# Kernel optimization log

Measured on AMD Instinct MI355X. Metric: run time of the kernel, lower is better.

## Reference

```python
import jax, jax.numpy as jnp
import numpy as np

N = 16384
E = 65536

def _nnconv(x, src, dst, edge_attr, A, b, root, bias, c_in, c_out):
    # edge MLP: [E,2] -> [E, c_in*c_out], ReLU
    W = jax.nn.relu(edge_attr @ A + b).reshape(E, c_in, c_out)
    # gather source features, per-edge matmul: [E,c_in] x [E,c_in,c_out] -> [E,c_out]
    msg = jnp.einsum('ei,eio->eo', x[src], W)
    # scatter-add to target nodes
    agg = jax.ops.segment_sum(msg, dst, num_segments=N)
    return agg + x @ root + bias

def setup_inputs() -> dict:
    key = jax.random.key(0)
    ks = jax.random.split(key, 12)
    inp = {
        'x': jax.random.normal(ks[0], (N, 8), dtype=jnp.float32),
        'edge_index': jax.random.randint(ks[1], (2, E), 0, N, dtype=jnp.int64),
        'edge_attr': jax.random.normal(ks[2], (E, 2), dtype=jnp.float32),
        # edge-MLP 1: Linear(2, 512)
        'A1': jax.random.normal(ks[3], (2, 512), dtype=jnp.float32) * (1.0 / np.sqrt(2.0)),
        'b1': jnp.zeros((512,), dtype=jnp.float32),
        # edge-MLP 2: Linear(2, 4096)
        'A2': jax.random.normal(ks[4], (2, 4096), dtype=jnp.float32) * (1.0 / np.sqrt(2.0)),
        'b2': jnp.zeros((4096,), dtype=jnp.float32),
        # NNConv root weights + biases
        'root1': jax.random.normal(ks[5], (8, 64), dtype=jnp.float32) * (1.0 / np.sqrt(8.0)),
        'bias1': jnp.zeros((64,), dtype=jnp.float32),
        'root2': jax.random.normal(ks[6], (64, 64), dtype=jnp.float32) * (1.0 / np.sqrt(64.0)),
        'bias2': jnp.zeros((64,), dtype=jnp.float32),
    }
    return inp

def reference(x, edge_index, edge_attr, A1, b1, A2, b2, root1, bias1, root2, bias2):
    src = edge_index[0]  # x_j (message source)
    dst = edge_index[1]  # aggregation target
    h = _nnconv(x, src, dst, edge_attr, A1, b1, root1, bias1, 8, 64)
    h = _nnconv(h, src, dst, edge_attr, A2, b2, root2, bias2, 64, 64)
    return h
```

## Files before the change

### kernel.cpp

```cpp
#include <hip/hip_runtime.h>

#define N_NODES 16384
#define N_EDGES 65536

typedef float f32x16 __attribute__((ext_vector_type(16)));
typedef float f32x8  __attribute__((ext_vector_type(8)));
typedef float f32x4  __attribute__((ext_vector_type(4)));
typedef float f32x2  __attribute__((ext_vector_type(2)));

__device__ __forceinline__ float rfl_f(float v) {
    int i = __builtin_amdgcn_readfirstlane(__builtin_bit_cast(int, v));
    return __builtin_bit_cast(float, i);
}

__global__ void k_node1(const float* __restrict__ x, const float* __restrict__ root1,
                        const float* __restrict__ bias1, float* __restrict__ h1) {
    int t = blockIdx.x * blockDim.x + threadIdx.x;
    int n = t >> 6, o = t & 63;
    float acc = bias1[o];
#pragma unroll
    for (int i = 0; i < 8; ++i)
        acc = fmaf(x[n * 8 + i], root1[i * 64 + o], acc);
    h1[t] = acc;
}

__global__ __launch_bounds__(256)
void k_edge1(const float* __restrict__ x, const int* __restrict__ ei,
             const float* __restrict__ ea, const float* __restrict__ A1,
             const float* __restrict__ b1, float* __restrict__ h1) {
    int lane = threadIdx.x & 63;
    f32x8 W0, W1, BB;
#pragma unroll
    for (int i = 0; i < 8; ++i) {
        W0[i] = A1[i * 64 + lane];
        W1[i] = A1[512 + i * 64 + lane];
        BB[i] = b1[i * 64 + lane];
    }
    asm volatile("" : "+v"(W0), "+v"(W1), "+v"(BB));

    int wid = blockIdx.x * (blockDim.x >> 6) + (threadIdx.x >> 6);
    int nw = gridDim.x * (blockDim.x >> 6);
#pragma clang loop unroll(disable)
    for (int p = wid; p < N_EDGES / 2; p += nw) {
        int2 srcp = ((const int2*)ei)[p];
        int2 dstp = ((const int2*)(ei + N_EDGES))[p];
        float4 eap = ((const float4*)ea)[p];
        int s0 = __builtin_amdgcn_readfirstlane(srcp.x);
        int s1 = __builtin_amdgcn_readfirstlane(srcp.y);
        int d0 = __builtin_amdgcn_readfirstlane(dstp.x);
        int d1 = __builtin_amdgcn_readfirstlane(dstp.y);
        f32x2 e00 = {rfl_f(eap.x), rfl_f(eap.x)};
        f32x2 e01 = {rfl_f(eap.y), rfl_f(eap.y)};
        f32x2 e10 = {rfl_f(eap.z), rfl_f(eap.z)};
        f32x2 e11 = {rfl_f(eap.w), rfl_f(eap.w)};
        const float* xp0 = x + (size_t)s0 * 8;
        const float* xp1 = x + (size_t)s1 * 8;
        f32x8 ha, hb;
        asm volatile("s_load_dwordx8 %0, %2, 0x0\n\t"
                     "s_load_dwordx8 %1, %3, 0x0\n\t"
                     "s_waitcnt lgkmcnt(0)"
                     : "=&s"(ha), "=&s"(hb) : "s"(xp0), "s"(xp1));
        f32x2 acc0 = {0.f, 0.f}, acc1 = {0.f, 0.f};
        const f32x2 z2 = {0.f, 0.f};
#pragma unroll
        for (int k = 0; k < 4; ++k) {
            f32x2 w0p = {W0[2 * k], W0[2 * k + 1]};
            f32x2 w1p = {W1[2 * k], W1[2 * k + 1]};
            f32x2 bp  = {BB[2 * k], BB[2 * k + 1]};
            f32x2 wv0 = __builtin_elementwise_max(
                __builtin_elementwise_fma(e01, w1p,
                    __builtin_elementwise_fma(e00, w0p, bp)), z2);
            f32x2 h0p = {ha[2 * k], ha[2 * k + 1]};
            acc0 = __builtin_elementwise_fma(h0p, wv0, acc0);
            f32x2 wv1 = __builtin_elementwise_max(
                __builtin_elementwise_fma(e11, w1p,
                    __builtin_elementwise_fma(e10, w0p, bp)), z2);
            f32x2 h1p = {hb[2 * k], hb[2 * k + 1]};
            acc1 = __builtin_elementwise_fma(h1p, wv1, acc1);
        }
        atomicAdd(&h1[(size_t)d0 * 64 + lane], acc0[0] + acc0[1]);
        atomicAdd(&h1[(size_t)d1 * 64 + lane], acc1[0] + acc1[1]);
    }
}

__global__ __launch_bounds__(256)
void k_node2(const float* __restrict__ h1, const float* __restrict__ root2,
             const float* __restrict__ bias2, float* __restrict__ out) {
    int lane = threadIdx.x & 63;
    f32x16 R0, R1, R2, R3;
#pragma unroll
    for (int i = 0; i < 16; ++i) {
        R0[i] = root2[(i)      * 64 + lane];
        R1[i] = root2[(16 + i) * 64 + lane];
        R2[i] = root2[(32 + i) * 64 + lane];
        R3[i] = root2[(48 + i) * 64 + lane];
    }
    asm volatile("" : "+v"(R0), "+v"(R1), "+v"(R2), "+v"(R3));
    float bias = bias2[lane];

    int wid = blockIdx.x * (blockDim.x >> 6) + (threadIdx.x >> 6);
    int nw = gridDim.x * (blockDim.x >> 6);
#pragma clang loop unroll(disable)
    for (int n = wid; n < N_NODES; n += nw) {
        int nu = __builtin_amdgcn_readfirstlane(n);
        const float* hp = h1 + (size_t)nu * 64;
        f32x16 h0, h1v, h2, h3;
        asm volatile("s_load_dwordx16 %0, %4, 0x0\n\t"
                     "s_load_dwordx16 %1, %4, 0x40\n\t"
                     "s_load_dwordx16 %2, %4, 0x80\n\t"
                     "s_load_dwordx16 %3, %4, 0xc0\n\t"
                     "s_waitcnt lgkmcnt(0)"
                     : "=&s"(h0), "=&s"(h1v), "=&s"(h2), "=&s"(h3) : "s"(hp));
        f32x2 accp = {bias, 0.f};
#pragma unroll
        for (int k = 0; k < 8; ++k) {
            f32x2 hp0 = {h0[2 * k], h0[2 * k + 1]};
            f32x2 rp0 = {R0[2 * k], R0[2 * k + 1]};
            accp = __builtin_elementwise_fma(hp0, rp0, accp);
            f32x2 hp1 = {h1v[2 * k], h1v[2 * k + 1]};
            f32x2 rp1 = {R1[2 * k], R1[2 * k + 1]};
            accp = __builtin_elementwise_fma(hp1, rp1, accp);
            f32x2 hp2 = {h2[2 * k], h2[2 * k + 1]};
            f32x2 rp2 = {R2[2 * k], R2[2 * k + 1]};
            accp = __builtin_elementwise_fma(hp2, rp2, accp);
            f32x2 hp3 = {h3[2 * k], h3[2 * k + 1]};
            f32x2 rp3 = {R3[2 * k], R3[2 * k + 1]};
            accp = __builtin_elementwise_fma(hp3, rp3, accp);
        }
        out[(size_t)nu * 64 + lane] = accp[0] + accp[1];
    }
}

__global__ __launch_bounds__(256, 3)
void k_edge2(const float* __restrict__ h1, const int* __restrict__ ei,
             const float* __restrict__ ea, const float* __restrict__ A2,
             const float* __restrict__ b2, float* __restrict__ out) {
    __shared__ __align__(16) float WT[3 * 64 * 36];
    int half = blockIdx.x & 1;
    for (int j = threadIdx.x; j < 2048; j += 256) {
        int i = j >> 6, o = j & 63;
        WT[o * 36 + i]               = A2[half * 2048 + j];
        WT[64 * 36 + o * 36 + i]     = A2[4096 + half * 2048 + j];
        WT[2 * 64 * 36 + o * 36 + i] = b2[half * 2048 + j];
    }
    __syncthreads();

    int lane = threadIdx.x & 63;
    int base = __builtin_amdgcn_readfirstlane(half * 32);
    unsigned laddr = (unsigned)(uintptr_t)WT + lane * 144;

    f32x4 wa[8], wb[8], wc[8];
    asm volatile(
        "ds_read_b128 %0, %12 offset:0\n\t"
        "ds_read_b128 %1, %12 offset:16\n\t"
        "ds_read_b128 %2, %12 offset:32\n\t"
        "ds_read_b128 %3, %12 offset:48\n\t"
        "ds_read_b128 %4, %12 offset:9216\n\t"
        "ds_read_b128 %5, %12 offset:9232\n\t"
        "ds_read_b128 %6, %12 offset:9248\n\t"
        "ds_read_b128 %7, %12 offset:9264\n\t"
        "ds_read_b128 %8, %12 offset:18432\n\t"
        "ds_read_b128 %9, %12 offset:18448\n\t"
        "ds_read_b128 %10, %12 offset:18464\n\t"
        "ds_read_b128 %11, %12 offset:18480"
        : "=&v"(wa[0]), "=&v"(wa[1]), "=&v"(wa[2]), "=&v"(wa[3]),
          "=&v"(wb[0]), "=&v"(wb[1]), "=&v"(wb[2]), "=&v"(wb[3]),
          "=&v"(wc[0]), "=&v"(wc[1]), "=&v"(wc[2]), "=&v"(wc[3])
        : "v"(laddr));
    asm volatile(
        "ds_read_b128 %0, %12 offset:64\n\t"
        "ds_read_b128 %1, %12 offset:80\n\t"
        "ds_read_b128 %2, %12 offset:96\n\t"
        "ds_read_b128 %3, %12 offset:112\n\t"
        "ds_read_b128 %4, %12 offset:9280\n\t"
        "ds_read_b128 %5, %12 offset:9296\n\t"
        "ds_read_b128 %6, %12 offset:9312\n\t"
        "ds_read_b128 %7, %12 offset:9328\n\t"
        "ds_read_b128 %8, %12 offset:18496\n\t"
        "ds_read_b128 %9, %12 offset:18512\n\t"
        "ds_read_b128 %10, %12 offset:18528\n\t"
        "ds_read_b128 %11, %12 offset:18544"
        : "=&v"(wa[4]), "=&v"(wa[5]), "=&v"(wa[6]), "=&v"(wa[7]),
          "=&v"(wb[4]), "=&v"(wb[5]), "=&v"(wb[6]), "=&v"(wb[7]),
          "=&v"(wc[4]), "=&v"(wc[5]), "=&v"(wc[6]), "=&v"(wc[7])
        : "v"(laddr));
    asm volatile("s_waitcnt lgkmcnt(0)"
        : "+v"(wa[0]), "+v"(wa[1]), "+v"(wa[2]), "+v"(wa[3]),
          "+v"(wa[4]), "+v"(wa[5]), "+v"(wa[6]), "+v"(wa[7]),
          "+v"(wb[0]), "+v"(wb[1]), "+v"(wb[2]), "+v"(wb[3]),
          "+v"(wb[4]), "+v"(wb[5]), "+v"(wb[6]), "+v"(wb[7]),
          "+v"(wc[0]), "+v"(wc[1]), "+v"(wc[2]), "+v"(wc[3]),
          "+v"(wc[4]), "+v"(wc[5]), "+v"(wc[6]), "+v"(wc[7]));

    int g = blockIdx.x >> 1;
    int wslot = g * 4 + (threadIdx.x >> 6);
    const int STRIDE = 1536;

    f32x16 ha, hb, hc, hd;

    int p0 = wslot;
    int2   dst_c = ((const int2*)(ei + N_EDGES))[p0];
    float4 ea_c  = ((const float4*)ea)[p0];
    {
        int2 src0 = ((const int2*)ei)[p0];
        int s0 = __builtin_amdgcn_readfirstlane(src0.x);
        int s1 = __builtin_amdgcn_readfirstlane(src0.y);
        const float* hp0 = h1 + (size_t)s0 * 64 + base;
        const float* hp1 = h1 + (size_t)s1 * 64 + base;
        asm volatile("s_load_dwordx16 %0, %4, 0x0\n\t"
                     "s_load_dwordx16 %1, %4, 0x40\n\t"
                     "s_load_dwordx16 %2, %5, 0x0\n\t"
                     "s_load_dwordx16 %3, %5, 0x40"
                     : "=&s"(ha), "=&s"(hb), "=&s"(hc), "=&s"(hd)
                     : "s"(hp0), "s"(hp1));
    }
    int pn = p0 + STRIDE; if (pn > N_EDGES / 2 - 1) pn = N_EDGES / 2 - 1;
    int2   src_n = ((const int2*)ei)[pn];
    int2   dst_n = ((const int2*)(ei + N_EDGES))[pn];
    float4 ea_n  = ((const float4*)ea)[pn];

#pragma clang loop unroll(disable)
    for (int p = wslot; p < N_EDGES / 2; p += STRIDE) {
        int s0n = __builtin_amdgcn_readfirstlane(src_n.x);
        int s1n = __builtin_amdgcn_readfirstlane(src_n.y);
        const float* hpn0 = h1 + (size_t)s0n * 64 + base;
        const float* hpn1 = h1 + (size_t)s1n * 64 + base;

        asm volatile("s_waitcnt lgkmcnt(0)"
            : "+s"(ha), "+s"(hb), "+s"(hc), "+s"(hd));

        f32x2 e00 = {ea_c.x, ea_c.x}, e01 = {ea_c.y, ea_c.y};
        f32x2 e10 = {ea_c.z, ea_c.z}, e11 = {ea_c.w, ea_c.w};
        const f32x2 z2 = {0.f, 0.f};
        f32x2 acc0 = z2, acc1 = z2;
#pragma unroll
        for (int q = 0; q < 4; ++q) {
#pragma unroll
            for (int k = 0; k < 2; ++k) {
                f32x2 w0p = {wa[q][2 * k], wa[q][2 * k + 1]};
                f32x2 w1p = {wb[q][2 * k], wb[q][2 * k + 1]};
                f32x2 bp  = {wc[q][2 * k], wc[q][2 * k + 1]};
                f32x2 wv0 = __builtin_elementwise_max(
                    __builtin_elementwise_fma(e01, w1p,
                        __builtin_elementwise_fma(e00, w0p, bp)), z2);
                f32x2 h0p = {ha[q * 4 + 2 * k], ha[q * 4 + 2 * k + 1]};
                acc0 = __builtin_elementwise_fma(h0p, wv0, acc0);
                f32x2 wv1 = __builtin_elementwise_max(
                    __builtin_elementwise_fma(e11, w1p,
                        __builtin_elementwise_fma(e10, w0p, bp)), z2);
                f32x2 h1p = {hc[q * 4 + 2 * k], hc[q * 4 + 2 * k + 1]};
                acc1 = __builtin_elementwise_fma(h1p, wv1, acc1);
            }
        }
        asm volatile("s_load_dwordx16 %0, %2, 0x0\n\t"
                     "s_load_dwordx16 %1, %3, 0x0"
                     : "=&s"(ha), "=&s"(hc) : "s"(hpn0), "s"(hpn1));
#pragma unroll
        for (int q = 4; q < 8; ++q) {
#pragma unroll
            for (int k = 0; k < 2; ++k) {
                f32x2 w0p = {wa[q][2 * k], wa[q][2 * k + 1]};
                f32x2 w1p = {wb[q][2 * k], wb[q][2 * k + 1]};
                f32x2 bp  = {wc[q][2 * k], wc[q][2 * k + 1]};
                f32x2 wv0 = __builtin_elementwise_max(
                    __builtin_elementwise_fma(e01, w1p,
                        __builtin_elementwise_fma(e00, w0p, bp)), z2);
                f32x2 h0p = {hb[(q - 4) * 4 + 2 * k], hb[(q - 4) * 4 + 2 * k + 1]};
                acc0 = __builtin_elementwise_fma(h0p, wv0, acc0);
                f32x2 wv1 = __builtin_elementwise_max(
                    __builtin_elementwise_fma(e11, w1p,
                        __builtin_elementwise_fma(e10, w0p, bp)), z2);
                f32x2 h1p = {hd[(q - 4) * 4 + 2 * k], hd[(q - 4) * 4 + 2 * k + 1]};
                acc1 = __builtin_elementwise_fma(h1p, wv1, acc1);
            }
        }
        asm volatile("s_load_dwordx16 %0, %2, 0x40\n\t"
                     "s_load_dwordx16 %1, %3, 0x40"
                     : "=&s"(hb), "=&s"(hd) : "s"(hpn0), "s"(hpn1));

        atomicAdd(&out[(size_t)dst_c.x * 64 + lane], acc0[0] + acc0[1]);
        atomicAdd(&out[(size_t)dst_c.y * 64 + lane], acc1[0] + acc1[1]);

        dst_c = dst_n; ea_c = ea_n;
        int pn2 = p + 2 * STRIDE; if (pn2 > N_EDGES / 2 - 1) pn2 = N_EDGES / 2 - 1;
        src_n = ((const int2*)ei)[pn2];
        dst_n = ((const int2*)(ei + N_EDGES))[pn2];
        ea_n  = ((const float4*)ea)[pn2];
    }
}

extern "C" void kernel_launch(void* const* d_in, const int* in_sizes, int n_in,
                              void* d_out, int out_size, void* d_ws, size_t ws_size,
                              hipStream_t stream) {
    const float* x     = (const float*)d_in[0];
    const int*   ei    = (const int*)d_in[1];
    const float* ea    = (const float*)d_in[2];
    const float* A1    = (const float*)d_in[3];
    const float* b1    = (const float*)d_in[4];
    const float* A2    = (const float*)d_in[5];
    const float* b2    = (const float*)d_in[6];
    const float* root1 = (const float*)d_in[7];
    const float* bias1 = (const float*)d_in[8];
    const float* root2 = (const float*)d_in[9];
    const float* bias2 = (const float*)d_in[10];
    float* out = (float*)d_out;
    float* h1  = (float*)d_ws;

    k_node1<<<N_NODES * 64 / 256, 256, 0, stream>>>(x, root1, bias1, h1);
    k_edge1<<<2048, 256, 0, stream>>>(x, ei, ea, A1, b1, h1);
    k_node2<<<1024, 256, 0, stream>>>(h1, root2, bias2, out);
    k_edge2<<<768, 256, 0, stream>>>(h1, ei, ea, A2, b2, out);
}
```

Measured before the change: 137.8 us.

## Software-pipeline edge1/node2 loads and split edge2 input channels into quarters

k_edge1 and k_node2 now prefetch the next iteration's indices and gathered scalar features before the current compute, so the scalar-load wait overlaps with arithmetic and atomics. k_edge2 splits the 64 input channels into four 16-channel slices per block instead of two 32-channel halves. This halves the per-wave weight registers and LDS footprint, drops the occupancy hint, and raises the grid to 2048 blocks. The price is twice as many atomic adds into the output and more redundant index and edge-attribute loads per edge.

```diff
diff --git a/kernel.cpp b/kernel.cpp
--- a/kernel.cpp
+++ b/kernel.cpp
@@ -40,28 +40,39 @@
 
     int wid = blockIdx.x * (blockDim.x >> 6) + (threadIdx.x >> 6);
     int nw = gridDim.x * (blockDim.x >> 6);
+
+    f32x8 ha, hb;
+    int p0 = wid;
+    int2   dst_c = ((const int2*)(ei + N_EDGES))[p0];
+    float4 ea_c  = ((const float4*)ea)[p0];
+    {
+        int2 s = ((const int2*)ei)[p0];
+        int s0 = __builtin_amdgcn_readfirstlane(s.x);
+        int s1 = __builtin_amdgcn_readfirstlane(s.y);
+        const float* xp0 = x + (size_t)s0 * 8;
+        const float* xp1 = x + (size_t)s1 * 8;
+        asm volatile("s_load_dwordx8 %0, %2, 0x0\n\t"
+                     "s_load_dwordx8 %1, %3, 0x0"
+                     : "=&s"(ha), "=&s"(hb) : "s"(xp0), "s"(xp1));
+    }
+    int pn = p0 + nw; if (pn > N_EDGES / 2 - 1) pn = N_EDGES / 2 - 1;
+    int2   src_n = ((const int2*)ei)[pn];
+    int2   dst_n = ((const int2*)(ei + N_EDGES))[pn];
+    float4 ea_n  = ((const float4*)ea)[pn];
+
 #pragma clang loop unroll(disable)
     for (int p = wid; p < N_EDGES / 2; p += nw) {
-        int2 srcp = ((const int2*)ei)[p];
-        int2 dstp = ((const int2*)(ei + N_EDGES))[p];
-        float4 eap = ((const float4*)ea)[p];
-        int s0 = __builtin_amdgcn_readfirstlane(srcp.x);
-        int s1 = __builtin_amdgcn_readfirstlane(srcp.y);
-        int d0 = __builtin_amdgcn_readfirstlane(dstp.x);
-        int d1 = __builtin_amdgcn_readfirstlane(dstp.y);
-        f32x2 e00 = {rfl_f(eap.x), rfl_f(eap.x)};
-        f32x2 e01 = {rfl_f(eap.y), rfl_f(eap.y)};
-        f32x2 e10 = {rfl_f(eap.z), rfl_f(eap.z)};
-        f32x2 e11 = {rfl_f(eap.w), rfl_f(eap.w)};
-        const float* xp0 = x + (size_t)s0 * 8;
-        const float* xp1 = x + (size_t)s1 * 8;
-        f32x8 ha, hb;
-        asm volatile("s_load_dwordx8 %0, %2, 0x0\n\t"
-                     "s_load_dwordx8 %1, %3, 0x0\n\t"
-                     "s_waitcnt lgkmcnt(0)"
-                     : "=&s"(ha), "=&s"(hb) : "s"(xp0), "s"(xp1));
-        f32x2 acc0 = {0.f, 0.f}, acc1 = {0.f, 0.f};
+        int s0n = __builtin_amdgcn_readfirstlane(src_n.x);
+        int s1n = __builtin_amdgcn_readfirstlane(src_n.y);
+        const float* xpn0 = x + (size_t)s0n * 8;
+        const float* xpn1 = x + (size_t)s1n * 8;
+
+        asm volatile("s_waitcnt lgkmcnt(0)" : "+s"(ha), "+s"(hb));
+
+        f32x2 e00 = {ea_c.x, ea_c.x}, e01 = {ea_c.y, ea_c.y};
+        f32x2 e10 = {ea_c.z, ea_c.z}, e11 = {ea_c.w, ea_c.w};
         const f32x2 z2 = {0.f, 0.f};
+        f32x2 acc0 = z2, acc1 = z2;
 #pragma unroll
         for (int k = 0; k < 4; ++k) {
             f32x2 w0p = {W0[2 * k], W0[2 * k + 1]};
@@ -78,8 +89,18 @@
             f32x2 h1p = {hb[2 * k], hb[2 * k + 1]};
             acc1 = __builtin_elementwise_fma(h1p, wv1, acc1);
         }
-        atomicAdd(&h1[(size_t)d0 * 64 + lane], acc0[0] + acc0[1]);
-        atomicAdd(&h1[(size_t)d1 * 64 + lane], acc1[0] + acc1[1]);
+        asm volatile("s_load_dwordx8 %0, %2, 0x0\n\t"
+                     "s_load_dwordx8 %1, %3, 0x0"
+                     : "=&s"(ha), "=&s"(hb) : "s"(xpn0), "s"(xpn1));
+
+        atomicAdd(&h1[(size_t)dst_c.x * 64 + lane], acc0[0] + acc0[1]);
+        atomicAdd(&h1[(size_t)dst_c.y * 64 + lane], acc1[0] + acc1[1]);
+
+        dst_c = dst_n; ea_c = ea_n;
+        int pn2 = p + 2 * nw; if (pn2 > N_EDGES / 2 - 1) pn2 = N_EDGES / 2 - 1;
+        src_n = ((const int2*)ei)[pn2];
+        dst_n = ((const int2*)(ei + N_EDGES))[pn2];
+        ea_n  = ((const float4*)ea)[pn2];
     }
 }
 
@@ -100,17 +121,25 @@
 
     int wid = blockIdx.x * (blockDim.x >> 6) + (threadIdx.x >> 6);
     int nw = gridDim.x * (blockDim.x >> 6);
-#pragma clang loop unroll(disable)
-    for (int n = wid; n < N_NODES; n += nw) {
-        int nu = __builtin_amdgcn_readfirstlane(n);
-        const float* hp = h1 + (size_t)nu * 64;
-        f32x16 h0, h1v, h2, h3;
+
+    f32x16 h0, h1v, h2, h3;
+    int nu_c = __builtin_amdgcn_readfirstlane(wid);
+    {
+        const float* hp = h1 + (size_t)nu_c * 64;
         asm volatile("s_load_dwordx16 %0, %4, 0x0\n\t"
                      "s_load_dwordx16 %1, %4, 0x40\n\t"
                      "s_load_dwordx16 %2, %4, 0x80\n\t"
-                     "s_load_dwordx16 %3, %4, 0xc0\n\t"
-                     "s_waitcnt lgkmcnt(0)"
+                     "s_load_dwordx16 %3, %4, 0xc0"
                      : "=&s"(h0), "=&s"(h1v), "=&s"(h2), "=&s"(h3) : "s"(hp));
+    }
+#pragma clang loop unroll(disable)
+    for (int n = wid; n < N_NODES; n += nw) {
+        int nn = n + nw; if (nn >= N_NODES) nn = n;
+        int nu_n = __builtin_amdgcn_readfirstlane(nn);
+        const float* hpn = h1 + (size_t)nu_n * 64;
+
+        asm volatile("s_waitcnt lgkmcnt(0)"
+                     : "+s"(h0), "+s"(h1v), "+s"(h2), "+s"(h3));
         f32x2 accp = {bias, 0.f};
 #pragma unroll
         for (int k = 0; k < 8; ++k) {
@@ -127,92 +156,75 @@
             f32x2 rp3 = {R3[2 * k], R3[2 * k + 1]};
             accp = __builtin_elementwise_fma(hp3, rp3, accp);
         }
-        out[(size_t)nu * 64 + lane] = accp[0] + accp[1];
-    }
-}
-
-__global__ __launch_bounds__(256, 3)
+        asm volatile("s_load_dwordx16 %0, %4, 0x0\n\t"
+                     "s_load_dwordx16 %1, %4, 0x40\n\t"
+                     "s_load_dwordx16 %2, %4, 0x80\n\t"
+                     "s_load_dwordx16 %3, %4, 0xc0"
+                     : "=&s"(h0), "=&s"(h1v), "=&s"(h2), "=&s"(h3) : "s"(hpn));
+        out[(size_t)nu_c * 64 + lane] = accp[0] + accp[1];
+        nu_c = nu_n;
+    }
+}
+
+__global__ __launch_bounds__(256)
 void k_edge2(const float* __restrict__ h1, const int* __restrict__ ei,
              const float* __restrict__ ea, const float* __restrict__ A2,
              const float* __restrict__ b2, float* __restrict__ out) {
-    __shared__ __align__(16) float WT[3 * 64 * 36];
-    int half = blockIdx.x & 1;
-    for (int j = threadIdx.x; j < 2048; j += 256) {
-        int i = j >> 6, o = j & 63;
-        WT[o * 36 + i]               = A2[half * 2048 + j];
-        WT[64 * 36 + o * 36 + i]     = A2[4096 + half * 2048 + j];
-        WT[2 * 64 * 36 + o * 36 + i] = b2[half * 2048 + j];
+    __shared__ __align__(16) float WT[3 * 64 * 20];
+    int q = blockIdx.x & 3;
+    for (int j = threadIdx.x; j < 1024; j += 256) {
+        int il = j >> 6, o = j & 63;
+        int ig = q * 16 + il;
+        WT[o * 20 + il]        = A2[ig * 64 + o];
+        WT[1280 + o * 20 + il] = A2[4096 + ig * 64 + o];
+        WT[2560 + o * 20 + il] = b2[ig * 64 + o];
     }
     __syncthreads();
 
     int lane = threadIdx.x & 63;
-    int base = __builtin_amdgcn_readfirstlane(half * 32);
-    unsigned laddr = (unsigned)(uintptr_t)WT + lane * 144;
-
-    f32x4 wa[8], wb[8], wc[8];
+    unsigned laddr = (unsigned)(uintptr_t)WT + lane * 80;
+
+    f32x4 wa[4], wb[4], wc[4];
     asm volatile(
         "ds_read_b128 %0, %12 offset:0\n\t"
         "ds_read_b128 %1, %12 offset:16\n\t"
         "ds_read_b128 %2, %12 offset:32\n\t"
         "ds_read_b128 %3, %12 offset:48\n\t"
-        "ds_read_b128 %4, %12 offset:9216\n\t"
-        "ds_read_b128 %5, %12 offset:9232\n\t"
-        "ds_read_b128 %6, %12 offset:9248\n\t"
-        "ds_read_b128 %7, %12 offset:9264\n\t"
-        "ds_read_b128 %8, %12 offset:18432\n\t"
-        "ds_read_b128 %9, %12 offset:18448\n\t"
-        "ds_read_b128 %10, %12 offset:18464\n\t"
-        "ds_read_b128 %11, %12 offset:18480"
+        "ds_read_b128 %4, %12 offset:5120\n\t"
+        "ds_read_b128 %5, %12 offset:5136\n\t"
+        "ds_read_b128 %6, %12 offset:5152\n\t"
+        "ds_read_b128 %7, %12 offset:5168\n\t"
+        "ds_read_b128 %8, %12 offset:10240\n\t"
+        "ds_read_b128 %9, %12 offset:10256\n\t"
+        "ds_read_b128 %10, %12 offset:10272\n\t"
+        "ds_read_b128 %11, %12 offset:10288"
         : "=&v"(wa[0]), "=&v"(wa[1]), "=&v"(wa[2]), "=&v"(wa[3]),
           "=&v"(wb[0]), "=&v"(wb[1]), "=&v"(wb[2]), "=&v"(wb[3]),
           "=&v"(wc[0]), "=&v"(wc[1]), "=&v"(wc[2]), "=&v"(wc[3])
         : "v"(laddr));
-    asm volatile(
-        "ds_read_b128 %0, %12 offset:64\n\t"
-        "ds_read_b128 %1, %12 offset:80\n\t"
-        "ds_read_b128 %2, %12 offset:96\n\t"
-        "ds_read_b128 %3, %12 offset:112\n\t"
-        "ds_read_b128 %4, %12 offset:9280\n\t"
-        "ds_read_b128 %5, %12 offset:9296\n\t"
-        "ds_read_b128 %6, %12 offset:9312\n\t"
-        "ds_read_b128 %7, %12 offset:9328\n\t"
-        "ds_read_b128 %8, %12 offset:18496\n\t"
-        "ds_read_b128 %9, %12 offset:18512\n\t"
-        "ds_read_b128 %10, %12 offset:18528\n\t"
-        "ds_read_b128 %11, %12 offset:18544"
-        : "=&v"(wa[4]), "=&v"(wa[5]), "=&v"(wa[6]), "=&v"(wa[7]),
-          "=&v"(wb[4]), "=&v"(wb[5]), "=&v"(wb[6]), "=&v"(wb[7]),
-          "=&v"(wc[4]), "=&v"(wc[5]), "=&v"(wc[6]), "=&v"(wc[7])
-        : "v"(laddr));
     asm volatile("s_waitcnt lgkmcnt(0)"
         : "+v"(wa[0]), "+v"(wa[1]), "+v"(wa[2]), "+v"(wa[3]),
-          "+v"(wa[4]), "+v"(wa[5]), "+v"(wa[6]), "+v"(wa[7]),
           "+v"(wb[0]), "+v"(wb[1]), "+v"(wb[2]), "+v"(wb[3]),
-          "+v"(wb[4]), "+v"(wb[5]), "+v"(wb[6]), "+v"(wb[7]),
-          "+v"(wc[0]), "+v"(wc[1]), "+v"(wc[2]), "+v"(wc[3]),
-          "+v"(wc[4]), "+v"(wc[5]), "+v"(wc[6]), "+v"(wc[7]));
-
-    int g = blockIdx.x >> 1;
+          "+v"(wc[0]), "+v"(wc[1]), "+v"(wc[2]), "+v"(wc[3]));
+
+    int base = q * 16;
+    int g = blockIdx.x >> 2;
     int wslot = g * 4 + (threadIdx.x >> 6);
-    const int STRIDE = 1536;
-
-    f32x16 ha, hb, hc, hd;
-
+    const int STRIDE = 2048;
+
+    f32x16 ha, hc;
     int p0 = wslot;
     int2   dst_c = ((const int2*)(ei + N_EDGES))[p0];
     float4 ea_c  = ((const float4*)ea)[p0];
     {
-        int2 src0 = ((const int2*)ei)[p0];
-        int s0 = __builtin_amdgcn_readfirstlane(src0.x);
-        int s1 = __builtin_amdgcn_readfirstlane(src0.y);
+        int2 s = ((const int2*)ei)[p0];
+        int s0 = __builtin_amdgcn_readfirstlane(s.x);
+        int s1 = __builtin_amdgcn_readfirstlane(s.y);
         const float* hp0 = h1 + (size_t)s0 * 64 + base;
         const float* hp1 = h1 + (size_t)s1 * 64 + base;
-        asm volatile("s_load_dwordx16 %0, %4, 0x0\n\t"
-                     "s_load_dwordx16 %1, %4, 0x40\n\t"
-                     "s_load_dwordx16 %2, %5, 0x0\n\t"
-                     "s_load_dwordx16 %3, %5, 0x40"
-                     : "=&s"(ha), "=&s"(hb), "=&s"(hc), "=&s"(hd)
-                     : "s"(hp0), "s"(hp1));
+        asm volatile("s_load_dwordx16 %0, %2, 0x0\n\t"
+                     "s_load_dwordx16 %1, %3, 0x0"
+                     : "=&s"(ha), "=&s"(hc) : "s"(hp0), "s"(hp1));
     }
     int pn = p0 + STRIDE; if (pn > N_EDGES / 2 - 1) pn = N_EDGES / 2 - 1;
     int2   src_n = ((const int2*)ei)[pn];
@@ -226,57 +238,34 @@
         const float* hpn0 = h1 + (size_t)s0n * 64 + base;
         const float* hpn1 = h1 + (size_t)s1n * 64 + base;
 
-        asm volatile("s_waitcnt lgkmcnt(0)"
-            : "+s"(ha), "+s"(hb), "+s"(hc), "+s"(hd));
+        asm volatile("s_waitcnt lgkmcnt(0)" : "+s"(ha), "+s"(hc));
 
         f32x2 e00 = {ea_c.x, ea_c.x}, e01 = {ea_c.y, ea_c.y};
         f32x2 e10 = {ea_c.z, ea_c.z}, e11 = {ea_c.w, ea_c.w};
         const f32x2 z2 = {0.f, 0.f};
         f32x2 acc0 = z2, acc1 = z2;
 #pragma unroll
-        for (int q = 0; q < 4; ++q) {
+        for (int qq = 0; qq < 4; ++qq) {
 #pragma unroll
             for (int k = 0; k < 2; ++k) {
-                f32x2 w0p = {wa[q][2 * k], wa[q][2 * k + 1]};
-                f32x2 w1p = {wb[q][2 * k], wb[q][2 * k + 1]};
-                f32x2 bp  = {wc[q][2 * k], wc[q][2 * k + 1]};
+                f32x2 w0p = {wa[qq][2 * k], wa[qq][2 * k + 1]};
+                f32x2 w1p = {wb[qq][2 * k], wb[qq][2 * k + 1]};
+                f32x2 bp  = {wc[qq][2 * k], wc[qq][2 * k + 1]};
                 f32x2 wv0 = __builtin_elementwise_max(
                     __builtin_elementwise_fma(e01, w1p,
                         __builtin_elementwise_fma(e00, w0p, bp)), z2);
-                f32x2 h0p = {ha[q * 4 + 2 * k], ha[q * 4 + 2 * k + 1]};
+                f32x2 h0p = {ha[qq * 4 + 2 * k], ha[qq * 4 + 2 * k + 1]};
                 acc0 = __builtin_elementwise_fma(h0p, wv0, acc0);
                 f32x2 wv1 = __builtin_elementwise_max(
                     __builtin_elementwise_fma(e11, w1p,
                         __builtin_elementwise_fma(e10, w0p, bp)), z2);
-                f32x2 h1p = {hc[q * 4 + 2 * k], hc[q * 4 + 2 * k + 1]};
+                f32x2 h1p = {hc[qq * 4 + 2 * k], hc[qq * 4 + 2 * k + 1]};
                 acc1 = __builtin_elementwise_fma(h1p, wv1, acc1);
             }
         }
         asm volatile("s_load_dwordx16 %0, %2, 0x0\n\t"
                      "s_load_dwordx16 %1, %3, 0x0"
                      : "=&s"(ha), "=&s"(hc) : "s"(hpn0), "s"(hpn1));
-#pragma unroll
-        for (int q = 4; q < 8; ++q) {
-#pragma unroll
-            for (int k = 0; k < 2; ++k) {
-                f32x2 w0p = {wa[q][2 * k], wa[q][2 * k + 1]};
-                f32x2 w1p = {wb[q][2 * k], wb[q][2 * k + 1]};
-                f32x2 bp  = {wc[q][2 * k], wc[q][2 * k + 1]};
-                f32x2 wv0 = __builtin_elementwise_max(
-                    __builtin_elementwise_fma(e01, w1p,
-                        __builtin_elementwise_fma(e00, w0p, bp)), z2);
-                f32x2 h0p = {hb[(q - 4) * 4 + 2 * k], hb[(q - 4) * 4 + 2 * k + 1]};
-                acc0 = __builtin_elementwise_fma(h0p, wv0, acc0);
-                f32x2 wv1 = __builtin_elementwise_max(
-                    __builtin_elementwise_fma(e11, w1p,
-                        __builtin_elementwise_fma(e10, w0p, bp)), z2);
-                f32x2 h1p = {hd[(q - 4) * 4 + 2 * k], hd[(q - 4) * 4 + 2 * k + 1]};
-                acc1 = __builtin_elementwise_fma(h1p, wv1, acc1);
-            }
-        }
-        asm volatile("s_load_dwordx16 %0, %2, 0x40\n\t"
-                     "s_load_dwordx16 %1, %3, 0x40"
-                     : "=&s"(hb), "=&s"(hd) : "s"(hpn0), "s"(hpn1));
 
         atomicAdd(&out[(size_t)dst_c.x * 64 + lane], acc0[0] + acc0[1]);
         atomicAdd(&out[(size_t)dst_c.y * 64 + lane], acc1[0] + acc1[1]);
@@ -309,5 +298,5 @@
     k_node1<<<N_NODES * 64 / 256, 256, 0, stream>>>(x, root1, bias1, h1);
     k_edge1<<<2048, 256, 0, stream>>>(x, ei, ea, A1, b1, h1);
     k_node2<<<1024, 256, 0, stream>>>(h1, root2, bias2, out);
-    k_edge2<<<768, 256, 0, stream>>>(h1, ei, ea, A2, b2, out);
-}
+    k_edge2<<<2048, 256, 0, stream>>>(h1, ei, ea, A2, b2, out);
+}
```

Measured after the change: 166.2 us. 1.21x slower.
